# Kernel optimization log

Hardware: AMD Instinct MI355X
Metric: run time of the kernel (lower is better)

Reference implementation:

```python
import jax, jax.numpy as jnp
import numpy as np

B, N, T, F = 16, 512, 24, 64


def setup_inputs() -> dict:
    key = jax.random.key(0)
    k1, k2, k3, k4 = jax.random.split(key, 4)
    ori_flow = jax.random.normal(k1, (B, N, T, F), dtype=jnp.float32)
    uncer = jax.random.normal(k2, (B, N, T, F), dtype=jnp.float32)
    spatial_embedding = jax.random.normal(k3, (N, F), dtype=jnp.float32)
    # nn.Linear(channels, channels, bias=False): y = x @ W.T, W: (out, in)
    W1 = jax.random.normal(k4, (F, F), dtype=jnp.float32) * (1.0 / np.sqrt(F))
    return {"ori_flow": ori_flow, "uncer": uncer,
            "spatial_embedding": spatial_embedding, "W1": W1}


def reference(ori_flow, uncer, spatial_embedding, W1):
    b, n, t, f = ori_flow.shape
    # (B, N, T, f) -> (B*T, N, f)
    x = ori_flow.transpose(0, 2, 1, 3).reshape(-1, n, f)
    u = uncer.transpose(0, 2, 1, 3).reshape(-1, n, f)
    # spatial embedding is identical across batch and time after expand/permute
    emb = jnp.broadcast_to(spatial_embedding, (b * t, n, f))
    h = jnp.concatenate([x, emb], axis=-1)            # (B*T, N, 2f)
    rel = jax.nn.relu(jnp.einsum('bnf,bmf->bnm', h, h))  # (B*T, N, N)
    rel = jax.nn.softmax(rel, axis=-1)                # dropout p=0 -> identity
    # sharing_paras=True: both branches use linear1 (no bias)
    of = jax.nn.relu(jnp.einsum('bnm,bmf->bnf', rel, x) @ W1.T)
    uf = jax.nn.relu(jnp.einsum('bnm,bmf->bnf', rel, u) @ W1.T)
    of = of.reshape(b, t, n, f).transpose(0, 2, 1, 3)  # (B, N, T, f)
    uf = uf.reshape(b, t, n, f).transpose(0, 2, 1, 3)
    return of, uf
```

## Files before the change

kernel.cpp:

```cpp
#include <hip/hip_runtime.h>
#include <hip/hip_bf16.h>

#define BB 16
#define NN 512
#define TT 24
#define FF 64
#define OUT_OFF ((size_t)BB*NN*TT*FF)

#define AIS 136
#define XTS 72
#define XTSZ 4672

typedef __attribute__((ext_vector_type(8))) short v8s;
typedef __attribute__((ext_vector_type(16))) float v16f;

union U16x8 { uint4 v; unsigned int u[4]; unsigned short s[8]; };

__device__ inline v16f mfma32(v8s a, v8s b, v16f c) {
    return __builtin_amdgcn_mfma_f32_32x32x16_bf16(a, b, c, 0, 0, 0);
}

__device__ inline unsigned int fbits(float x) {
    union { float f; unsigned int u; } c; c.f = x; return c.u;
}
__device__ inline float ibits(unsigned int u) {
    union { float f; unsigned int u; } c; c.u = u; return c.f;
}
__device__ inline unsigned short f2bf_r(float x) {
    return (unsigned short)((fbits(x) + 0x8000u) >> 16);
}
__device__ inline unsigned int pkbf(float a, float b) {
    unsigned int r;
    asm("v_cvt_pk_bf16_f32 %0, %1, %2" : "=v"(r) : "v"(a), "v"(b));
    return r;
}
__device__ inline void split8(const float* f, U16x8& H, U16x8& L) {
    #pragma unroll
    for (int k = 0; k < 4; ++k) {
        unsigned int hp = pkbf(f[2*k], f[2*k+1]);
        float h0 = ibits(hp << 16);
        float h1 = ibits(hp & 0xffff0000u);
        L.u[k] = pkbf(f[2*k] - h0, f[2*k+1] - h1);
        H.u[k] = hp;
    }
}
__device__ inline void cvt8h(const float* f, U16x8& H) {
    #pragma unroll
    for (int k = 0; k < 8; ++k) H.s[k] = f2bf_r(f[k]);
}

__device__ inline v8s pfrag(const float* cr, int c) {
    unsigned int a0 = pkbf(cr[8*c+0], cr[8*c+1]);
    unsigned int a1 = pkbf(cr[8*c+2], cr[8*c+3]);
    unsigned int b0 = pkbf(cr[8*c+4], cr[8*c+5]);
    unsigned int b1 = pkbf(cr[8*c+6], cr[8*c+7]);
    asm("v_permlane32_swap_b32 %0, %1" : "+v"(a0), "+v"(b0));
    asm("v_permlane32_swap_b32 %0, %1" : "+v"(a1), "+v"(b1));
    union { v8s v; unsigned int u[4]; } P;
    P.u[0] = a0; P.u[1] = a1; P.u[2] = b0; P.u[3] = b1;
    return P.v;
}

__global__ __launch_bounds__(256, 2)
void spag_kernel(const float* __restrict__ ori, const float* __restrict__ unc,
                 const float* __restrict__ emb, const float* __restrict__ W1,
                 float* __restrict__ out)
{
    __shared__ __align__(16) unsigned short SH[2*64*AIS + 2*XTSZ];
    unsigned short* AjH = SH;
    unsigned short* AjL = SH + 64*AIS;
    unsigned short* XT  = SH + 2*64*AIS;
    unsigned short* UT  = XT + XTSZ;

    const int tid  = threadIdx.x;
    const int xcd  = blockIdx.x & 7;
    const int slot = blockIdx.x >> 3;
    const int bt   = xcd * 48 + (slot >> 2);
    const int it   = slot & 3;
    const int b    = bt / TT, t = bt % TT;
    const int i0   = it * 128;

    const int lane = tid & 63;
    const int w    = tid >> 6;
    const int m    = lane & 31;
    const int hi   = lane >> 5;

    const int pj  = tid >> 3;
    const int f0  = (tid & 7) * 8;
    const int jme = 2 * pj;

    float pa0[8], pa1[8], pu0[8], pu1[8];
    {
        const size_t r0 = ((size_t)((b*NN + jme)*TT + t))*FF + f0;
        const size_t r1 = r0 + (size_t)TT*FF;
        *(float4*)&pa0[0] = *(const float4*)(ori + r0);
        *(float4*)&pa0[4] = *(const float4*)(ori + r0 + 4);
        *(float4*)&pa1[0] = *(const float4*)(ori + r1);
        *(float4*)&pa1[4] = *(const float4*)(ori + r1 + 4);
        *(float4*)&pu0[0] = *(const float4*)(unc + r0);
        *(float4*)&pu0[4] = *(const float4*)(unc + r0 + 4);
        *(float4*)&pu1[0] = *(const float4*)(unc + r1);
        *(float4*)&pu1[4] = *(const float4*)(unc + r1 + 4);
    }

    v8s bH[8], bL[8];
    #pragma unroll
    for (int p = 0; p < 2; ++p) {
        {
            const int sr = tid >> 2, fc = (tid & 3) * 16;
            const float* xb = ori + ((size_t)((b*NN + i0 + p*64 + sr)*TT + t))*FF + fc;
            const float* eb = emb + (size_t)(i0 + p*64 + sr)*FF + fc;
            float tf[8]; U16x8 H, L;
            #pragma unroll
            for (int h = 0; h < 2; ++h) {
                *(float4*)&tf[0] = ((const float4*)xb)[2*h];
                *(float4*)&tf[4] = ((const float4*)xb)[2*h+1];
                split8(tf, H, L);
                *(uint4*)&AjH[sr*AIS + fc + h*8] = H.v;
                *(uint4*)&AjL[sr*AIS + fc + h*8] = L.v;
                *(float4*)&tf[0] = ((const float4*)eb)[2*h];
                *(float4*)&tf[4] = ((const float4*)eb)[2*h+1];
                split8(tf, H, L);
                *(uint4*)&AjH[sr*AIS + 64 + fc + h*8] = H.v;
                *(uint4*)&AjL[sr*AIS + 64 + fc + h*8] = L.v;
            }
        }
        __syncthreads();
        if ((w >> 1) == p) {
            const int lr = (w & 1)*32 + m;
            #pragma unroll
            for (int kk = 0; kk < 8; ++kk) {
                bH[kk] = *(const v8s*)&AjH[lr*AIS + kk*16 + hi*8];
                bL[kk] = *(const v8s*)&AjL[lr*AIS + kk*16 + hi*8];
            }
        }
        __syncthreads();
    }

    v16f accX0 = (v16f)(0.0f), accX1 = (v16f)(0.0f);
    v16f accU0 = (v16f)(0.0f), accU1 = (v16f)(0.0f);
    float rs    = 0.0f;
    float m_run = 0.0f;

    for (int jt = 0; jt < 8; ++jt) {
        const int j0 = jt * 64;
        __syncthreads();

        float t0[8], t1[8];
        {
            const float* e0 = emb + (size_t)(j0 + jme)*FF + f0;
            *(float4*)&t0[0] = *(const float4*)(e0);
            *(float4*)&t0[4] = *(const float4*)(e0 + 4);
            *(float4*)&t1[0] = *(const float4*)(e0 + FF);
            *(float4*)&t1[4] = *(const float4*)(e0 + FF + 4);

            U16x8 H0, L0, H1, L1;
            split8(pa0, H0, L0); split8(pa1, H1, L1);
            *(uint4*)&AjH[ jme   *AIS + f0] = H0.v;
            *(uint4*)&AjH[(jme+1)*AIS + f0] = H1.v;
            *(uint4*)&AjL[ jme   *AIS + f0] = L0.v;
            *(uint4*)&AjL[(jme+1)*AIS + f0] = L1.v;
        }
        __syncthreads();

        {
            U16x8 H0, L0, H1, L1;
            split8(t0, H0, L0); split8(t1, H1, L1);
            *(uint4*)&AjH[ jme   *AIS + 64 + f0] = H0.v;
            *(uint4*)&AjH[(jme+1)*AIS + 64 + f0] = H1.v;
            *(uint4*)&AjL[ jme   *AIS + 64 + f0] = L0.v;
            *(uint4*)&AjL[(jme+1)*AIS + 64 + f0] = L1.v;
            #pragma unroll
            for (int k = 0; k < 8; ++k) {
                int f = f0 + k;
                int off = f*XTS + (f>>4)*16 + jme;
                *(unsigned int*)&XT[off] = pkbf(pa0[k], pa1[k]);
                *(unsigned int*)&UT[off] = pkbf(pu0[k], pu1[k]);
            }
        }
        v16f C0 = (v16f)(0.0f), C1 = (v16f)(0.0f);
        #pragma unroll
        for (int kk = 0; kk < 4; ++kk) {
            const int fo = kk*16 + hi*8;
            v8s aH0 = *(const v8s*)&AjH[ m     *AIS + fo];
            v8s aL0 = *(const v8s*)&AjL[ m     *AIS + fo];
            v8s aH1 = *(const v8s*)&AjH[(32+m)*AIS + fo];
            v8s aL1 = *(const v8s*)&AjL[(32+m)*AIS + fo];
            C0 = mfma32(aH0, bH[kk], C0);
            C1 = mfma32(aH1, bH[kk], C1);
            C0 = mfma32(aH0, bL[kk], C0);
            C1 = mfma32(aH1, bL[kk], C1);
            C0 = mfma32(aL0, bH[kk], C0);
            C1 = mfma32(aL1, bH[kk], C1);
        }
        __syncthreads();

        if (jt < 7) {
            const size_t r0 = ((size_t)((b*NN + j0 + 64 + jme)*TT + t))*FF + f0;
            const size_t r1 = r0 + (size_t)TT*FF;
            *(float4*)&pa0[0] = *(const float4*)(ori + r0);
            *(float4*)&pa0[4] = *(const float4*)(ori + r0 + 4);
            *(float4*)&pa1[0] = *(const float4*)(ori + r1);
            *(float4*)&pa1[4] = *(const float4*)(ori + r1 + 4);
            *(float4*)&pu0[0] = *(const float4*)(unc + r0);
            *(float4*)&pu0[4] = *(const float4*)(unc + r0 + 4);
            *(float4*)&pu1[0] = *(const float4*)(unc + r1);
            *(float4*)&pu1[4] = *(const float4*)(unc + r1 + 4);
        }

        #pragma unroll
        for (int kk = 4; kk < 8; ++kk) {
            const int fo = kk*16 + hi*8;
            v8s aH0 = *(const v8s*)&AjH[ m     *AIS + fo];
            v8s aL0 = *(const v8s*)&AjL[ m     *AIS + fo];
            v8s aH1 = *(const v8s*)&AjH[(32+m)*AIS + fo];
            v8s aL1 = *(const v8s*)&AjL[(32+m)*AIS + fo];
            C0 = mfma32(aH0, bH[kk], C0);
            C1 = mfma32(aH1, bH[kk], C1);
            C0 = mfma32(aH0, bL[kk], C0);
            C1 = mfma32(aH1, bL[kk], C1);
            C0 = mfma32(aL0, bH[kk], C0);
            C1 = mfma32(aL1, bH[kk], C1);
        }

        float mt = 0.0f;
        #pragma unroll
        for (int r = 0; r < 16; ++r) {
            float s0 = fmaxf(C0[r], 0.0f); C0[r] = s0;
            float s1 = fmaxf(C1[r], 0.0f); C1[r] = s1;
            mt = fmaxf(mt, fmaxf(s0, s1));
        }
        mt = fmaxf(mt, __shfl_xor(mt, 32));
        if (!__all(mt <= m_run + 8.0f)) {
            float m_new = fmaxf(m_run, mt);
            float al = __expf(m_run - m_new);
            rs *= al; m_run = m_new;
            #pragma unroll
            for (int r = 0; r < 16; ++r) {
                float a = __shfl(al, (r & 3) + 8*(r >> 2) + 4*hi);
                accX0[r] *= a; accX1[r] *= a;
                accU0[r] *= a; accU1[r] *= a;
            }
        }

        v8s P[4];
        {
            float cr[16];
            #pragma unroll
            for (int r = 0; r < 16; ++r) {
                float e = __expf(C0[r] - m_run);
                cr[r] = e;
                rs += e;
            }
            P[0] = pfrag(cr, 0);
            P[1] = pfrag(cr, 1);
            #pragma unroll
            for (int r = 0; r < 16; ++r) {
                float e = __expf(C1[r] - m_run);
                cr[r] = e;
                rs += e;
            }
            P[2] = pfrag(cr, 0);
            P[3] = pfrag(cr, 1);
        }

        #pragma unroll
        for (int kk = 0; kk < 4; ++kk) {
            const int fo = kk*16 + hi*8;
            v8s bx0 = *(const v8s*)&XT[ m     *XTS + (( m    )>>4)*16 + fo];
            v8s bu0 = *(const v8s*)&UT[ m     *XTS + (( m    )>>4)*16 + fo];
            v8s bx1 = *(const v8s*)&XT[(32+m)*XTS + (((32+m))>>4)*16 + fo];
            v8s bu1 = *(const v8s*)&UT[(32+m)*XTS + (((32+m))>>4)*16 + fo];
            accX0 = mfma32(P[kk], bx0, accX0);
            accX1 = mfma32(P[kk], bx1, accX1);
            accU0 = mfma32(P[kk], bu0, accU0);
            accU1 = mfma32(P[kk], bu1, accU1);
        }
    }

    __syncthreads();
    rs += __shfl_xor(rs, 32);
    float inv = 1.0f / rs;

    unsigned short* Ox = SH;
    unsigned short* Ou = SH + 128*XTS;
    unsigned short* Wt = SH + 256*XTS;

    #pragma unroll
    for (int r = 0; r < 16; ++r) {
        int il = (r & 3) + 8*(r >> 2) + 4*hi;
        float iv = __shfl(inv, il);
        int row = w*32 + il;
        Ox[row*XTS + m]      = f2bf_r(accX0[r] * iv);
        Ox[row*XTS + 32 + m] = f2bf_r(accX1[r] * iv);
        Ou[row*XTS + m]      = f2bf_r(accU0[r] * iv);
        Ou[row*XTS + 32 + m] = f2bf_r(accU1[r] * iv);
    }
    {
        const int sr = tid >> 2, fc = (tid & 3) * 16;
        const float* wb = W1 + sr*FF + fc;
        float tf[8]; U16x8 H;
        #pragma unroll
        for (int h = 0; h < 2; ++h) {
            *(float4*)&tf[0] = ((const float4*)wb)[2*h];
            *(float4*)&tf[4] = ((const float4*)wb)[2*h+1];
            cvt8h(tf, H);
            *(uint4*)&Wt[sr*XTS + fc + h*8] = H.v;
        }
    }
    __syncthreads();

    v8s ao[4], aq[4];
    #pragma unroll
    for (int kk = 0; kk < 4; ++kk) {
        const int fo = kk*16 + hi*8;
        ao[kk] = *(const v8s*)&Ox[(w*32 + m)*XTS + fo];
        aq[kk] = *(const v8s*)&Ou[(w*32 + m)*XTS + fo];
    }
    #pragma unroll
    for (int ot = 0; ot < 2; ++ot) {
        v16f ax = (v16f)(0.0f), au = (v16f)(0.0f);
        #pragma unroll
        for (int kk = 0; kk < 4; ++kk) {
            const int fo = kk*16 + hi*8;
            v8s bw = *(const v8s*)&Wt[(ot*32 + m)*XTS + fo];
            ax = mfma32(ao[kk], bw, ax);
            au = mfma32(aq[kk], bw, au);
        }
        #pragma unroll
        for (int r = 0; r < 16; ++r) {
            int il = (r & 3) + 8*(r >> 2) + 4*hi;
            int i = i0 + w*32 + il;
            int o = ot*32 + m;
            size_t idx = ((size_t)((b*NN + i)*TT + t))*FF + o;
            out[idx]           = fmaxf(ax[r], 0.0f);
            out[OUT_OFF + idx] = fmaxf(au[r], 0.0f);
        }
    }
}

extern "C" void kernel_launch(void* const* d_in, const int* in_sizes, int n_in,
                              void* d_out, int out_size, void* d_ws, size_t ws_size,
                              hipStream_t stream) {
    const float* ori = (const float*)d_in[0];
    const float* unc = (const float*)d_in[1];
    const float* emb = (const float*)d_in[2];
    const float* W1  = (const float*)d_in[3];
    float* out = (float*)d_out;

    spag_kernel<<<dim3(BB*TT*4), dim3(256), 0, stream>>>(ori, unc, emb, W1, out);
}
```

Baseline: 255.3 us.

## Defer P·V MFMAs to next iteration and use native exp2 with log2e prescale

The P·V MFMA block for each key tile is moved into the next iteration, before the barrier that precedes the overwrite of XT/UT. A final drain after the loop handles the last tile. The aim is to overlap those MFMAs with the next tile's global loads and LDS staging instead of running them serially after the softmax. Separately, the query-side operand is pre-multiplied by log2(e) so the softmax can use the raw v_exp_f32 (exp2) instruction rather than __expf. This changes the bf16 rounding of the scaled operand slightly and makes the rescale threshold of 8 act in log2 units.

New measurement: 259.0 us. No clear change (+1.5%).

```diff
diff --git a/kernel.cpp b/kernel.cpp
--- a/kernel.cpp
+++ b/kernel.cpp
@@ -10,6 +10,7 @@
 #define AIS 136
 #define XTS 72
 #define XTSZ 4672
+#define LOG2E 1.4426950408889634f
 
 typedef __attribute__((ext_vector_type(8))) short v8s;
 typedef __attribute__((ext_vector_type(16))) float v16f;
@@ -28,6 +29,11 @@
 }
 __device__ inline unsigned short f2bf_r(float x) {
     return (unsigned short)((fbits(x) + 0x8000u) >> 16);
+}
+__device__ inline float ex2(float x) {
+    float r;
+    asm("v_exp_f32 %0, %1" : "=v"(r) : "v"(x));
+    return r;
 }
 __device__ inline unsigned int pkbf(float a, float b) {
     unsigned int r;
@@ -115,11 +121,15 @@
             for (int h = 0; h < 2; ++h) {
                 *(float4*)&tf[0] = ((const float4*)xb)[2*h];
                 *(float4*)&tf[4] = ((const float4*)xb)[2*h+1];
+                #pragma unroll
+                for (int k = 0; k < 8; ++k) tf[k] *= LOG2E;
                 split8(tf, H, L);
                 *(uint4*)&AjH[sr*AIS + fc + h*8] = H.v;
                 *(uint4*)&AjL[sr*AIS + fc + h*8] = L.v;
                 *(float4*)&tf[0] = ((const float4*)eb)[2*h];
                 *(float4*)&tf[4] = ((const float4*)eb)[2*h+1];
+                #pragma unroll
+                for (int k = 0; k < 8; ++k) tf[k] *= LOG2E;
                 split8(tf, H, L);
                 *(uint4*)&AjH[sr*AIS + 64 + fc + h*8] = H.v;
                 *(uint4*)&AjL[sr*AIS + 64 + fc + h*8] = L.v;
@@ -141,6 +151,7 @@
     v16f accU0 = (v16f)(0.0f), accU1 = (v16f)(0.0f);
     float rs    = 0.0f;
     float m_run = 0.0f;
+    v8s Pv[4];
 
     for (int jt = 0; jt < 8; ++jt) {
         const int j0 = jt * 64;
@@ -160,6 +171,20 @@
             *(uint4*)&AjH[(jme+1)*AIS + f0] = H1.v;
             *(uint4*)&AjL[ jme   *AIS + f0] = L0.v;
             *(uint4*)&AjL[(jme+1)*AIS + f0] = L1.v;
+        }
+        if (jt > 0) {
+            #pragma unroll
+            for (int kk = 0; kk < 4; ++kk) {
+                const int fo = kk*16 + hi*8;
+                v8s bx0 = *(const v8s*)&XT[ m     *XTS + (( m    )>>4)*16 + fo];
+                v8s bu0 = *(const v8s*)&UT[ m     *XTS + (( m    )>>4)*16 + fo];
+                v8s bx1 = *(const v8s*)&XT[(32+m)*XTS + (((32+m))>>4)*16 + fo];
+                v8s bu1 = *(const v8s*)&UT[(32+m)*XTS + (((32+m))>>4)*16 + fo];
+                accX0 = mfma32(Pv[kk], bx0, accX0);
+                accX1 = mfma32(Pv[kk], bx1, accX1);
+                accU0 = mfma32(Pv[kk], bu0, accU0);
+                accU1 = mfma32(Pv[kk], bu1, accU1);
+            }
         }
         __syncthreads();
 
@@ -233,7 +258,7 @@
         mt = fmaxf(mt, __shfl_xor(mt, 32));
         if (!__all(mt <= m_run + 8.0f)) {
             float m_new = fmaxf(m_run, mt);
-            float al = __expf(m_run - m_new);
+            float al = ex2(m_run - m_new);
             rs *= al; m_run = m_new;
             #pragma unroll
             for (int r = 0; r < 16; ++r) {
@@ -243,39 +268,38 @@
             }
         }
 
-        v8s P[4];
         {
             float cr[16];
             #pragma unroll
             for (int r = 0; r < 16; ++r) {
-                float e = __expf(C0[r] - m_run);
+                float e = ex2(C0[r] - m_run);
                 cr[r] = e;
                 rs += e;
             }
-            P[0] = pfrag(cr, 0);
-            P[1] = pfrag(cr, 1);
+            Pv[0] = pfrag(cr, 0);
+            Pv[1] = pfrag(cr, 1);
             #pragma unroll
             for (int r = 0; r < 16; ++r) {
-                float e = __expf(C1[r] - m_run);
+                float e = ex2(C1[r] - m_run);
                 cr[r] = e;
                 rs += e;
             }
-            P[2] = pfrag(cr, 0);
-            P[3] = pfrag(cr, 1);
-        }
-
-        #pragma unroll
-        for (int kk = 0; kk < 4; ++kk) {
-            const int fo = kk*16 + hi*8;
-            v8s bx0 = *(const v8s*)&XT[ m     *XTS + (( m    )>>4)*16 + fo];
-            v8s bu0 = *(const v8s*)&UT[ m     *XTS + (( m    )>>4)*16 + fo];
-            v8s bx1 = *(const v8s*)&XT[(32+m)*XTS + (((32+m))>>4)*16 + fo];
-            v8s bu1 = *(const v8s*)&UT[(32+m)*XTS + (((32+m))>>4)*16 + fo];
-            accX0 = mfma32(P[kk], bx0, accX0);
-            accX1 = mfma32(P[kk], bx1, accX1);
-            accU0 = mfma32(P[kk], bu0, accU0);
-            accU1 = mfma32(P[kk], bu1, accU1);
-        }
+            Pv[2] = pfrag(cr, 0);
+            Pv[3] = pfrag(cr, 1);
+        }
+    }
+
+    #pragma unroll
+    for (int kk = 0; kk < 4; ++kk) {
+        const int fo = kk*16 + hi*8;
+        v8s bx0 = *(const v8s*)&XT[ m     *XTS + (( m    )>>4)*16 + fo];
+        v8s bu0 = *(const v8s*)&UT[ m     *XTS + (( m    )>>4)*16 + fo];
+        v8s bx1 = *(const v8s*)&XT[(32+m)*XTS + (((32+m))>>4)*16 + fo];
+        v8s bu1 = *(const v8s*)&UT[(32+m)*XTS + (((32+m))>>4)*16 + fo];
+        accX0 = mfma32(Pv[kk], bx0, accX0);
+        accX1 = mfma32(Pv[kk], bx1, accX1);
+        accU0 = mfma32(Pv[kk], bu0, accU0);
+        accU1 = mfma32(Pv[kk], bu1, accU1);
     }
 
     __syncthreads();
```

## Pipeline next key tile's LDS writes into current iteration and use exp2 softmax

Applied to the files above, without the earlier changes.

Moves the split-and-store of the next j-tile's ori rows into the tail of the current iteration, after the second half of the QK MFMAs, so one of the two per-iteration barriers disappears. The embedding rows for the next tile are prefetched with the ori/uncer loads. The query-side operand is prescaled by log2(e) so the softmax can call the raw v_exp_f32 instead of __expf. This trades a shorter barrier chain for more live registers and depends on the LDS reuse ordering being correct, and it changes the threshold semantics of the max-rescale check (it now operates in log2 units).

Result: no change. 260.3 us (+2.0%).

```diff
diff --git a/kernel.cpp b/kernel.cpp
--- a/kernel.cpp
+++ b/kernel.cpp
@@ -10,6 +10,7 @@
 #define AIS 136
 #define XTS 72
 #define XTSZ 4672
+#define LOG2E 1.4426950408889634f
 
 typedef __attribute__((ext_vector_type(8))) short v8s;
 typedef __attribute__((ext_vector_type(16))) float v16f;
@@ -28,6 +29,11 @@
 }
 __device__ inline unsigned short f2bf_r(float x) {
     return (unsigned short)((fbits(x) + 0x8000u) >> 16);
+}
+__device__ inline float ex2(float x) {
+    float r;
+    asm("v_exp_f32 %0, %1" : "=v"(r) : "v"(x));
+    return r;
 }
 __device__ inline unsigned int pkbf(float a, float b) {
     unsigned int r;
@@ -115,11 +121,15 @@
             for (int h = 0; h < 2; ++h) {
                 *(float4*)&tf[0] = ((const float4*)xb)[2*h];
                 *(float4*)&tf[4] = ((const float4*)xb)[2*h+1];
+                #pragma unroll
+                for (int k = 0; k < 8; ++k) tf[k] *= LOG2E;
                 split8(tf, H, L);
                 *(uint4*)&AjH[sr*AIS + fc + h*8] = H.v;
                 *(uint4*)&AjL[sr*AIS + fc + h*8] = L.v;
                 *(float4*)&tf[0] = ((const float4*)eb)[2*h];
                 *(float4*)&tf[4] = ((const float4*)eb)[2*h+1];
+                #pragma unroll
+                for (int k = 0; k < 8; ++k) tf[k] *= LOG2E;
                 split8(tf, H, L);
                 *(uint4*)&AjH[sr*AIS + 64 + fc + h*8] = H.v;
                 *(uint4*)&AjL[sr*AIS + 64 + fc + h*8] = L.v;
@@ -136,6 +146,23 @@
         }
         __syncthreads();
     }
+
+    float t0[8], t1[8];
+    {
+        const float* e0 = emb + (size_t)jme*FF + f0;
+        *(float4*)&t0[0] = *(const float4*)(e0);
+        *(float4*)&t0[4] = *(const float4*)(e0 + 4);
+        *(float4*)&t1[0] = *(const float4*)(e0 + FF);
+        *(float4*)&t1[4] = *(const float4*)(e0 + FF + 4);
+
+        U16x8 H0, L0, H1, L1;
+        split8(pa0, H0, L0); split8(pa1, H1, L1);
+        *(uint4*)&AjH[ jme   *AIS + f0] = H0.v;
+        *(uint4*)&AjH[(jme+1)*AIS + f0] = H1.v;
+        *(uint4*)&AjL[ jme   *AIS + f0] = L0.v;
+        *(uint4*)&AjL[(jme+1)*AIS + f0] = L1.v;
+    }
+    __syncthreads();
 
     v16f accX0 = (v16f)(0.0f), accX1 = (v16f)(0.0f);
     v16f accU0 = (v16f)(0.0f), accU1 = (v16f)(0.0f);
@@ -144,24 +171,6 @@
 
     for (int jt = 0; jt < 8; ++jt) {
         const int j0 = jt * 64;
-        __syncthreads();
-
-        float t0[8], t1[8];
-        {
-            const float* e0 = emb + (size_t)(j0 + jme)*FF + f0;
-            *(float4*)&t0[0] = *(const float4*)(e0);
-            *(float4*)&t0[4] = *(const float4*)(e0 + 4);
-            *(float4*)&t1[0] = *(const float4*)(e0 + FF);
-            *(float4*)&t1[4] = *(const float4*)(e0 + FF + 4);
-
-            U16x8 H0, L0, H1, L1;
-            split8(pa0, H0, L0); split8(pa1, H1, L1);
-            *(uint4*)&AjH[ jme   *AIS + f0] = H0.v;
-            *(uint4*)&AjH[(jme+1)*AIS + f0] = H1.v;
-            *(uint4*)&AjL[ jme   *AIS + f0] = L0.v;
-            *(uint4*)&AjL[(jme+1)*AIS + f0] = L1.v;
-        }
-        __syncthreads();
 
         {
             U16x8 H0, L0, H1, L1;
@@ -206,6 +215,11 @@
             *(float4*)&pu0[4] = *(const float4*)(unc + r0 + 4);
             *(float4*)&pu1[0] = *(const float4*)(unc + r1);
             *(float4*)&pu1[4] = *(const float4*)(unc + r1 + 4);
+            const float* e0 = emb + (size_t)(j0 + 64 + jme)*FF + f0;
+            *(float4*)&t0[0] = *(const float4*)(e0);
+            *(float4*)&t0[4] = *(const float4*)(e0 + 4);
+            *(float4*)&t1[0] = *(const float4*)(e0 + FF);
+            *(float4*)&t1[4] = *(const float4*)(e0 + FF + 4);
         }
 
         #pragma unroll
@@ -223,6 +237,15 @@
             C1 = mfma32(aL1, bH[kk], C1);
         }
 
+        if (jt < 7) {
+            U16x8 H0, L0, H1, L1;
+            split8(pa0, H0, L0); split8(pa1, H1, L1);
+            *(uint4*)&AjH[ jme   *AIS + f0] = H0.v;
+            *(uint4*)&AjH[(jme+1)*AIS + f0] = H1.v;
+            *(uint4*)&AjL[ jme   *AIS + f0] = L0.v;
+            *(uint4*)&AjL[(jme+1)*AIS + f0] = L1.v;
+        }
+
         float mt = 0.0f;
         #pragma unroll
         for (int r = 0; r < 16; ++r) {
@@ -233,7 +256,7 @@
         mt = fmaxf(mt, __shfl_xor(mt, 32));
         if (!__all(mt <= m_run + 8.0f)) {
             float m_new = fmaxf(m_run, mt);
-            float al = __expf(m_run - m_new);
+            float al = ex2(m_run - m_new);
             rs *= al; m_run = m_new;
             #pragma unroll
             for (int r = 0; r < 16; ++r) {
@@ -248,7 +271,7 @@
             float cr[16];
             #pragma unroll
             for (int r = 0; r < 16; ++r) {
-                float e = __expf(C0[r] - m_run);
+                float e = ex2(C0[r] - m_run);
                 cr[r] = e;
                 rs += e;
             }
@@ -256,7 +279,7 @@
             P[1] = pfrag(cr, 1);
             #pragma unroll
             for (int r = 0; r < 16; ++r) {
-                float e = __expf(C1[r] - m_run);
+                float e = ex2(C1[r] - m_run);
                 cr[r] = e;
                 rs += e;
             }
@@ -276,9 +299,9 @@
             accU0 = mfma32(P[kk], bu0, accU0);
             accU1 = mfma32(P[kk], bu1, accU1);
         }
-    }
-
-    __syncthreads();
+        __syncthreads();
+    }
+
     rs += __shfl_xor(rs, 32);
     float inv = 1.0f / rs;
 
```
